# Kernel tuning notes

Hardware: AMD Instinct MI355X
Metric: run time of the kernel (lower is better)

## Reference

```python
import jax, jax.numpy as jnp
import numpy as np

EMB_DIM = 1024
N_HEAD = 16
HEAD_SIZE = 64
B = 2
T = 2048


def setup_inputs() -> dict:
    key = jax.random.key(0)
    k_x, k_qkv, k_pw, k_pb = jax.random.split(key, 4)
    x = jax.random.normal(k_x, (B, T, EMB_DIM), dtype=jnp.float32)
    # nn.Linear(emb_dim, 3*emb_dim, bias=False): y = x @ W_qkv, W_qkv: [C, 3C]
    W_qkv = jax.random.normal(k_qkv, (EMB_DIM, 3 * EMB_DIM), dtype=jnp.float32) * (EMB_DIM ** -0.5)
    # nn.Linear(emb_dim, emb_dim) with bias
    W_proj = jax.random.normal(k_pw, (EMB_DIM, EMB_DIM), dtype=jnp.float32) * (EMB_DIM ** -0.5)
    b_proj = jax.random.normal(k_pb, (EMB_DIM,), dtype=jnp.float32) * 0.01
    return {"x": x, "W_qkv": W_qkv, "W_proj": W_proj, "b_proj": b_proj}


def reference(x, W_qkv, W_proj, b_proj):
    Bn, Tn, C = x.shape
    qkv = x @ W_qkv                          # [B, T, 3C]
    q, k, v = jnp.split(qkv, 3, axis=-1)
    # [B, T, H, D] -> attention over heads via einsum (no explicit transpose)
    q = q.reshape(Bn, Tn, N_HEAD, HEAD_SIZE)
    k = k.reshape(Bn, Tn, N_HEAD, HEAD_SIZE)
    v = v.reshape(Bn, Tn, N_HEAD, HEAD_SIZE)
    att = jnp.einsum("bthd,bshd->bhts", q, k) * (HEAD_SIZE ** -0.5)  # [B, H, T, T]
    causal = jnp.tril(jnp.ones((Tn, Tn), dtype=bool))
    att = jnp.where(causal, att, -jnp.inf)
    att = jax.nn.softmax(att, axis=-1)
    y = jnp.einsum("bhts,bshd->bthd", att, v).reshape(Bn, Tn, C)
    return y @ W_proj + b_proj
```

## Files before the change

kernel.cpp:

```cpp
#include <hip/hip_runtime.h>
#include <hip/hip_bf16.h>

typedef unsigned short u16;
typedef unsigned int u32;
typedef u16 u16x4 __attribute__((ext_vector_type(4)));
typedef u16 u16x8 __attribute__((ext_vector_type(8)));
typedef u32 u32x4 __attribute__((ext_vector_type(4)));
typedef __bf16 bf16x8 __attribute__((ext_vector_type(8)));
typedef float f32x4 __attribute__((ext_vector_type(4)));

__device__ __forceinline__ u16 f2bf(float f) {
  union { float f; unsigned u; } v; v.f = f;
  unsigned r = v.u + 0x7fffu + ((v.u >> 16) & 1u);
  return (u16)(r >> 16);
}

__device__ __forceinline__ u16 bf(float f) {
  __bf16 h = (__bf16)f;
  union { __bf16 h; u16 u; } c; c.h = h;
  return c.u;
}

__device__ __forceinline__ u32 pack2(float lo, float hi) {
  return (u32)bf(lo) | ((u32)bf(hi) << 16);
}

__device__ __forceinline__ float fexp2(float x) {
#if __has_builtin(__builtin_amdgcn_exp2f)
  return __builtin_amdgcn_exp2f(x);
#else
  return exp2f(x);
#endif
}

__device__ __forceinline__ float frcp(float x) {
#if __has_builtin(__builtin_amdgcn_rcpf)
  return __builtin_amdgcn_rcpf(x);
#else
  return 1.0f / x;
#endif
}

__device__ __forceinline__ void gload16(const void* g, void* l) {
  __builtin_amdgcn_global_load_lds((const __attribute__((address_space(1))) void*)g,
                                   (__attribute__((address_space(3))) void*)l, 16, 0, 0);
}

__global__ __launch_bounds__(256) void cvt_bf16(const float* __restrict__ in,
                                                u16* __restrict__ out, int n) {
  int i = (blockIdx.x * 256 + threadIdx.x) * 8;
  if (i >= n) return;
  f32x4 a = *(const f32x4*)(in + i);
  f32x4 b = *(const f32x4*)(in + i + 4);
  u16x8 r;
  r[0] = f2bf(a[0]); r[1] = f2bf(a[1]); r[2] = f2bf(a[2]); r[3] = f2bf(a[3]);
  r[4] = f2bf(b[0]); r[5] = f2bf(b[1]); r[6] = f2bf(b[2]); r[7] = f2bf(b[3]);
  *(u16x8*)(out + i) = r;
}

__global__ __launch_bounds__(256) void transpose_w(
    const float* __restrict__ Wqkv, const float* __restrict__ Wproj,
    u16* __restrict__ wqT, u16* __restrict__ wpT)
{
  __shared__ float tile[32][33];
  int bx = blockIdx.x;
  const float* in;
  u16* out;
  int N;
  if (bx < 96) { in = Wqkv; out = wqT; N = 3072; }
  else         { in = Wproj; out = wpT; N = 1024; bx -= 96; }
  const int K = 1024;
  int n0 = bx * 32, k0 = blockIdx.y * 32;
  int tx = threadIdx.x & 31, ty = threadIdx.x >> 5;
  for (int i = 0; i < 32; i += 8)
    tile[ty + i][tx] = in[(long)(k0 + ty + i) * N + n0 + tx];
  __syncthreads();
  for (int i = 0; i < 32; i += 8)
    out[(long)(n0 + ty + i) * K + k0 + tx] = f2bf(tile[tx][ty + i]);
}

template<int BM, int BN, bool F32OUT>
__global__ __launch_bounds__(256) void gemm_bt(
    const u16* __restrict__ A, const u16* __restrict__ Bt,
    void* __restrict__ Cp, const float* __restrict__ bias,
    int M, int N, int K)
{
  constexpr int MR = BM / 32, NR = BN / 32;
  constexpr int RA = BM / 32, RB = BN / 32;
  __shared__ char lds[(BM + BN) * 128];
  char* As = lds;
  char* Bs = lds + BM * 128;
  const int tid = threadIdx.x;
  const int l = tid & 63, w = tid >> 6;
  const int wr = w >> 1, wc = w & 1;
  const int lr = l & 15, q4 = l >> 4;
  const long row0 = (long)blockIdx.x * BM;
  const long col0 = (long)blockIdx.y * BN;

  f32x4 acc[MR][NR] = {};

  const u16* gA[RA];
  int oA[RA];
  for (int i = 0; i < RA; ++i) {
    int cc = i * 256 + tid;
    int r = cc >> 3, c = (cc & 7) ^ (r & 7);
    oA[i] = cc * 16;
    gA[i] = A + (row0 + r) * K + c * 8;
  }
  const u16* gB[RB];
  int oB[RB];
  for (int i = 0; i < RB; ++i) {
    int cc = i * 256 + tid;
    int r = cc >> 3, c = (cc & 7) ^ (r & 7);
    oB[i] = cc * 16;
    gB[i] = Bt + (col0 + r) * K + c * 8;
  }

  for (int k0 = 0; k0 < K; k0 += 64) {
    __syncthreads();
    for (int i = 0; i < RA; ++i) gload16(gA[i] + k0, As + oA[i]);
    for (int i = 0; i < RB; ++i) gload16(gB[i] + k0, Bs + oB[i]);
    __syncthreads();
    for (int kk = 0; kk < 2; ++kk) {
      bf16x8 a[MR], b[NR];
      for (int m = 0; m < MR; ++m) {
        int r = wr * (BM / 2) + m * 16 + lr;
        a[m] = *(const bf16x8*)(As + r * 128 + (((kk * 4 + q4) ^ (r & 7)) << 4));
      }
      for (int n = 0; n < NR; ++n) {
        int r = wc * (BN / 2) + n * 16 + lr;
        b[n] = *(const bf16x8*)(Bs + r * 128 + (((kk * 4 + q4) ^ (r & 7)) << 4));
      }
      for (int m = 0; m < MR; ++m)
        for (int n = 0; n < NR; ++n)
          acc[m][n] = __builtin_amdgcn_mfma_f32_16x16x32_bf16(a[m], b[n], acc[m][n], 0, 0, 0);
    }
  }

  for (int n = 0; n < NR; ++n) {
    int col = (int)col0 + wc * (BN / 2) + n * 16 + lr;
    float bv = 0.f;
    if (F32OUT) bv = bias[col];
    for (int m = 0; m < MR; ++m) {
      for (int reg = 0; reg < 4; ++reg) {
        long row = row0 + wr * (BM / 2) + m * 16 + q4 * 4 + reg;
        float vv = acc[m][n][reg] + bv;
        if (F32OUT) ((float*)Cp)[row * N + col] = vv;
        else        ((u16*)Cp)[row * N + col] = f2bf(vv);
      }
    }
  }
}

#define FXOR(d) (((((d) & 7) ^ (((d) >> 3) & 7))) << 4)

#define VSCAT(vtb, ra, rb)                                                     \
  for (int j = 0; j < 4; ++j) {                                                \
    int d = vd0 + j;                                                           \
    *(u32*)((vtb) + d * 128 + (vcol2 ^ FXOR(d))) = (u32)(ra)[j] | ((u32)(rb)[j] << 16); \
  }

#define COMPUTE_TILE(T)                                                        \
  if (64 * (T) <= wrow + 15) {                                                 \
    char* ks_ = ksmem + ((T) & 3) * 8192;                                      \
    char* vt_ = vtmem + ((T) & 3) * 8192;                                      \
    const int k0_ = 64 * (T);                                                  \
    f32x4 st[4] = {};                                                          \
    __builtin_amdgcn_s_setprio(1);                                             \
    for (int kk = 0; kk < 2; ++kk)                                             \
      for (int n = 0; n < 4; ++n) {                                            \
        int r = n * 16 + lr;                                                   \
        int c = (kk * 4 + g) ^ (r & 7);                                        \
        bf16x8 kf = *(const bf16x8*)(ks_ + r * 128 + (c << 4));                \
        st[n] = __builtin_amdgcn_mfma_f32_16x16x32_bf16(kf, qf[kk], st[n], 0, 0, 0); \
      }                                                                        \
    __builtin_amdgcn_s_setprio(0);                                             \
    if (k0_ + 63 > wrow) {                                                     \
      for (int n = 0; n < 4; ++n)                                              \
        for (int reg = 0; reg < 4; ++reg)                                      \
          if (k0_ + n * 16 + g * 4 + reg > wrow + lr)                          \
            st[n][reg] = -__builtin_inff();                                    \
    }                                                                          \
    float pm = fmaxf(fmaxf(fmaxf(st[0][0], st[0][1]), fmaxf(st[0][2], st[0][3])), \
                     fmaxf(fmaxf(st[1][0], st[1][1]), fmaxf(st[1][2], st[1][3]))); \
    pm = fmaxf(pm, fmaxf(fmaxf(fmaxf(st[2][0], st[2][1]), fmaxf(st[2][2], st[2][3])), \
                         fmaxf(fmaxf(st[3][0], st[3][1]), fmaxf(st[3][2], st[3][3])))); \
    pm = fmaxf(pm, __shfl_xor(pm, 16));                                        \
    pm = fmaxf(pm, __shfl_xor(pm, 32));                                        \
    if (__any(pm > mrun + 8.f)) {                                              \
      float mn = fmaxf(mrun, pm);                                              \
      float scl = fexp2(mrun - mn);                                            \
      mrun = mn;                                                               \
      lsum *= scl;                                                             \
      for (int n = 0; n < 4; ++n)                                              \
        for (int reg = 0; reg < 4; ++reg) o[n][reg] *= scl;                    \
    }                                                                          \
    float psum = 0.f;                                                          \
    u32 pk[4][2];                                                              \
    for (int n = 0; n < 4; ++n) {                                              \
      float p0 = fexp2(st[n][0] - mrun), p1 = fexp2(st[n][1] - mrun);          \
      float p2 = fexp2(st[n][2] - mrun), p3 = fexp2(st[n][3] - mrun);          \
      psum += (p0 + p1) + (p2 + p3);                                           \
      pk[n][0] = pack2(p0, p1);                                                \
      pk[n][1] = pack2(p2, p3);                                                \
    }                                                                          \
    lsum += psum;                                                              \
    __builtin_amdgcn_s_setprio(1);                                             \
    for (int kt = 0; kt < 2; ++kt) {                                           \
      u32x4 pb;                                                                \
      pb[0] = pk[2 * kt][0]; pb[1] = pk[2 * kt][1];                            \
      pb[2] = pk[2 * kt + 1][0]; pb[3] = pk[2 * kt + 1][1];                    \
      bf16x8 pf = *(bf16x8*)&pb;                                               \
      for (int n = 0; n < 4; ++n) {                                            \
        int dd = n * 16 + lr;                                                  \
        bf16x8 vf = *(const bf16x8*)(vt_ + dd * 128 + ((kt * 64 + g * 16) ^ FXOR(dd))); \
        o[n] = __builtin_amdgcn_mfma_f32_16x16x32_bf16(vf, pf, o[n], 0, 0, 0); \
      }                                                                        \
    }                                                                          \
    __builtin_amdgcn_s_setprio(0);                                             \
  }

__global__ __launch_bounds__(512) void attn_fwd(
    const u16* __restrict__ qkv, u16* __restrict__ atty)
{
  __shared__ char ksmem[4 * 8192];
  __shared__ char vtmem[4 * 8192];
  const int tid = threadIdx.x;
  const int l = tid & 63, w = tid >> 6;
  const int lr = l & 15, g = l >> 4;
  const int h = blockIdx.y;
  const int ti = blockIdx.x;
  const long base = (long)blockIdx.z * 2048;
  const int wrow = (w < 4) ? (ti * 64 + w * 16) : ((31 - ti) * 64 + (w - 4) * 16);

  bf16x8 qf[2];
  for (int kk = 0; kk < 2; ++kk) {
    u16x8 raw = *(const u16x8*)(qkv + (base + wrow + lr) * 3072 + h * 64 + kk * 32 + g * 8);
    u16x8 sc;
    for (int j = 0; j < 8; ++j) {
      union { unsigned u; float f; } c; c.u = ((unsigned)raw[j]) << 16;
      sc[j] = bf(c.f * 0.18033688f);
    }
    qf[kk] = *(bf16x8*)&sc;
  }

  float mrun = -__builtin_inff(), lsum = 0.f;
  f32x4 o[4] = {};

  const int kr = tid >> 3, kc = (tid & 7) ^ (kr & 7);
  const u16* kg = qkv + (base + kr) * 3072 + 1024 + h * 64 + kc * 8;
  const int va = tid >> 4;
  const int vd0 = (tid & 15) * 4;
  const int vk0 = va * 2;
  const int vn = vk0 >> 4, vgp2 = (vk0 >> 2) & 3, vr = vk0 & 3;
  const int vcol2 = ((vn >> 1) * 32 + vgp2 * 8 + (vn & 1) * 4 + vr) * 2;
  const u16* vgp = qkv + (base + vk0) * 3072 + 2048 + h * 64 + vd0;

  const int nkv = 32 - ti;

  {
    u16x4 a0 = *(const u16x4*)(vgp);
    u16x4 b0 = *(const u16x4*)(vgp + 3072);
    u16x4 a1 = *(const u16x4*)(vgp + 196608);
    u16x4 b1 = *(const u16x4*)(vgp + 196608 + 3072);
    gload16(kg, ksmem + tid * 16);
    gload16(kg + 196608, ksmem + 8192 + tid * 16);
    VSCAT(vtmem, a0, b0);
    VSCAT(vtmem + 8192, a1, b1);
  }
  __syncthreads();

  for (int tb = 0; tb < nkv; tb += 2) {
    u16x4 p2a, p2b, p3a, p3b;
    const bool pf2 = (tb + 2) < nkv, pf3 = (tb + 3) < nkv;
    if (pf2) {
      long off = (long)(tb + 2) * 196608;
      p2a = *(const u16x4*)(vgp + off);
      p2b = *(const u16x4*)(vgp + off + 3072);
      gload16(kg + off, ksmem + ((tb + 2) & 3) * 8192 + tid * 16);
    }
    if (pf3) {
      long off = (long)(tb + 3) * 196608;
      p3a = *(const u16x4*)(vgp + off);
      p3b = *(const u16x4*)(vgp + off + 3072);
      gload16(kg + off, ksmem + ((tb + 3) & 3) * 8192 + tid * 16);
    }

    COMPUTE_TILE(tb);
    if (tb + 1 < nkv) COMPUTE_TILE(tb + 1);

    if (pf2) VSCAT(vtmem + ((tb + 2) & 3) * 8192, p2a, p2b);
    if (pf3) VSCAT(vtmem + ((tb + 3) & 3) * 8192, p3a, p3b);
    __syncthreads();
  }

  lsum += __shfl_xor(lsum, 16);
  lsum += __shfl_xor(lsum, 32);
  float inv = frcp(lsum);
  long row = base + wrow + lr;
  for (int n = 0; n < 4; ++n) {
    u16x4 ov;
    for (int reg = 0; reg < 4; ++reg) ov[reg] = bf(o[n][reg] * inv);
    *(u16x4*)(atty + row * 1024 + h * 64 + n * 16 + g * 4) = ov;
  }
}

extern "C" void kernel_launch(void* const* d_in, const int* in_sizes, int n_in,
                              void* d_out, int out_size, void* d_ws, size_t ws_size,
                              hipStream_t stream) {
  const float* x     = (const float*)d_in[0];
  const float* Wqkv  = (const float*)d_in[1];
  const float* Wproj = (const float*)d_in[2];
  const float* bproj = (const float*)d_in[3];
  char* ws = (char*)d_ws;
  u16* xb   = (u16*)(ws);
  u16* wqT  = (u16*)(ws + 8388608);
  u16* wpT  = (u16*)(ws + 14680064);
  u16* qkv  = (u16*)(ws + 16777216);
  u16* atty = (u16*)(ws + 41943040);

  cvt_bf16<<<2048, 256, 0, stream>>>(x, xb, 4194304);
  transpose_w<<<dim3(128, 32), 256, 0, stream>>>(Wqkv, Wproj, wqT, wpT);
  gemm_bt<128, 128, false><<<dim3(32, 24), 256, 0, stream>>>(xb, wqT, (void*)qkv, nullptr, 4096, 3072, 1024);
  attn_fwd<<<dim3(16, 16, 2), 512, 0, stream>>>(qkv, atty);
  gemm_bt<128, 64, true><<<dim3(32, 16), 256, 0, stream>>>(atty, wpT, d_out, bproj, 4096, 1024, 1024);
}
```

Measured before the change: 114.0 us.

## Switch attention kernel to 32x32x16 MFMA with 4 waves of 32 query rows

Rewrites the flash-attention inner loop to use 32x32x16 bf16 MFMA instead of 16x16x32, with each wave owning 32 query rows and the block shrinking from 8 to 4 waves. K and V staging is widened so each thread loads two K rows and eight V columns, and the V scatter permutation is rebuilt to match the new fragment layout. The aim is fewer MFMA issues and less LDS fragment traffic per FLOP. In exchange each wave holds more registers, and fewer waves per block can reduce latency hiding.

```diff
diff --git a/kernel.cpp b/kernel.cpp
--- a/kernel.cpp
+++ b/kernel.cpp
@@ -8,6 +8,7 @@
 typedef u32 u32x4 __attribute__((ext_vector_type(4)));
 typedef __bf16 bf16x8 __attribute__((ext_vector_type(8)));
 typedef float f32x4 __attribute__((ext_vector_type(4)));
+typedef float f32x16 __attribute__((ext_vector_type(16)));
 
 __device__ __forceinline__ u16 f2bf(float f) {
   union { float f; unsigned u; } v; v.f = f;
@@ -155,135 +156,158 @@
 #define FXOR(d) (((((d) & 7) ^ (((d) >> 3) & 7))) << 4)
 
 #define VSCAT(vtb, ra, rb)                                                     \
-  for (int j = 0; j < 4; ++j) {                                                \
+  _Pragma("unroll")                                                            \
+  for (int j = 0; j < 8; ++j) {                                                \
     int d = vd0 + j;                                                           \
     *(u32*)((vtb) + d * 128 + (vcol2 ^ FXOR(d))) = (u32)(ra)[j] | ((u32)(rb)[j] << 16); \
   }
 
 #define COMPUTE_TILE(T)                                                        \
-  if (64 * (T) <= wrow + 15) {                                                 \
+  if ((T) <= tw) {                                                             \
     char* ks_ = ksmem + ((T) & 3) * 8192;                                      \
     char* vt_ = vtmem + ((T) & 3) * 8192;                                      \
-    const int k0_ = 64 * (T);                                                  \
-    f32x4 st[4] = {};                                                          \
+    f32x16 st[2] = {};                                                         \
     __builtin_amdgcn_s_setprio(1);                                             \
-    for (int kk = 0; kk < 2; ++kk)                                             \
-      for (int n = 0; n < 4; ++n) {                                            \
-        int r = n * 16 + lr;                                                   \
-        int c = (kk * 4 + g) ^ (r & 7);                                        \
-        bf16x8 kf = *(const bf16x8*)(ks_ + r * 128 + (c << 4));                \
-        st[n] = __builtin_amdgcn_mfma_f32_16x16x32_bf16(kf, qf[kk], st[n], 0, 0, 0); \
+    _Pragma("unroll")                                                          \
+    for (int w2 = 0; w2 < 2; ++w2) {                                           \
+      _Pragma("unroll")                                                        \
+      for (int sub = 0; sub < 4; ++sub) {                                      \
+        int r = w2 * 32 + lq;                                                  \
+        bf16x8 kf = *(const bf16x8*)(ks_ + r * 128 + (((sub * 2 + hi) ^ (r & 7)) << 4)); \
+        st[w2] = __builtin_amdgcn_mfma_f32_32x32x16_bf16(kf, qf[sub], st[w2], 0, 0, 0); \
       }                                                                        \
+    }                                                                          \
     __builtin_amdgcn_s_setprio(0);                                             \
-    if (k0_ + 63 > wrow) {                                                     \
-      for (int n = 0; n < 4; ++n)                                              \
-        for (int reg = 0; reg < 4; ++reg)                                      \
-          if (k0_ + n * 16 + g * 4 + reg > wrow + lr)                          \
-            st[n][reg] = -__builtin_inff();                                    \
-    }                                                                          \
-    float pm = fmaxf(fmaxf(fmaxf(st[0][0], st[0][1]), fmaxf(st[0][2], st[0][3])), \
-                     fmaxf(fmaxf(st[1][0], st[1][1]), fmaxf(st[1][2], st[1][3]))); \
-    pm = fmaxf(pm, fmaxf(fmaxf(fmaxf(st[2][0], st[2][1]), fmaxf(st[2][2], st[2][3])), \
-                         fmaxf(fmaxf(st[3][0], st[3][1]), fmaxf(st[3][2], st[3][3])))); \
-    pm = fmaxf(pm, __shfl_xor(pm, 16));                                        \
+    if ((T) == tw) {                                                           \
+      const int ro = (wrow & 32) + lq;                                         \
+      _Pragma("unroll")                                                        \
+      for (int w2 = 0; w2 < 2; ++w2)                                           \
+        _Pragma("unroll")                                                      \
+        for (int r = 0; r < 16; ++r)                                           \
+          if (w2 * 32 + (r & 3) + 8 * (r >> 2) + 4 * hi > ro)                  \
+            st[w2][r] = -__builtin_inff();                                     \
+    }                                                                          \
+    float pm = st[0][0];                                                       \
+    _Pragma("unroll")                                                          \
+    for (int r = 1; r < 16; ++r) pm = fmaxf(pm, st[0][r]);                     \
+    _Pragma("unroll")                                                          \
+    for (int r = 0; r < 16; ++r) pm = fmaxf(pm, st[1][r]);                     \
     pm = fmaxf(pm, __shfl_xor(pm, 32));                                        \
     if (__any(pm > mrun + 8.f)) {                                              \
       float mn = fmaxf(mrun, pm);                                              \
       float scl = fexp2(mrun - mn);                                            \
       mrun = mn;                                                               \
       lsum *= scl;                                                             \
-      for (int n = 0; n < 4; ++n)                                              \
-        for (int reg = 0; reg < 4; ++reg) o[n][reg] *= scl;                    \
-    }                                                                          \
+      _Pragma("unroll")                                                        \
+      for (int w2 = 0; w2 < 2; ++w2)                                           \
+        _Pragma("unroll")                                                      \
+        for (int r = 0; r < 16; ++r) o[w2][r] *= scl;                          \
+    }                                                                          \
+    u32 pk[2][8];                                                              \
     float psum = 0.f;                                                          \
-    u32 pk[4][2];                                                              \
-    for (int n = 0; n < 4; ++n) {                                              \
-      float p0 = fexp2(st[n][0] - mrun), p1 = fexp2(st[n][1] - mrun);          \
-      float p2 = fexp2(st[n][2] - mrun), p3 = fexp2(st[n][3] - mrun);          \
-      psum += (p0 + p1) + (p2 + p3);                                           \
-      pk[n][0] = pack2(p0, p1);                                                \
-      pk[n][1] = pack2(p2, p3);                                                \
+    _Pragma("unroll")                                                          \
+    for (int w2 = 0; w2 < 2; ++w2) {                                           \
+      _Pragma("unroll")                                                        \
+      for (int i2 = 0; i2 < 8; ++i2) {                                         \
+        float p0 = fexp2(st[w2][2 * i2] - mrun);                               \
+        float p1 = fexp2(st[w2][2 * i2 + 1] - mrun);                           \
+        psum += p0 + p1;                                                       \
+        pk[w2][i2] = pack2(p0, p1);                                            \
+      }                                                                        \
     }                                                                          \
     lsum += psum;                                                              \
     __builtin_amdgcn_s_setprio(1);                                             \
-    for (int kt = 0; kt < 2; ++kt) {                                           \
-      u32x4 pb;                                                                \
-      pb[0] = pk[2 * kt][0]; pb[1] = pk[2 * kt][1];                            \
-      pb[2] = pk[2 * kt + 1][0]; pb[3] = pk[2 * kt + 1][1];                    \
-      bf16x8 pf = *(bf16x8*)&pb;                                               \
-      for (int n = 0; n < 4; ++n) {                                            \
-        int dd = n * 16 + lr;                                                  \
-        bf16x8 vf = *(const bf16x8*)(vt_ + dd * 128 + ((kt * 64 + g * 16) ^ FXOR(dd))); \
-        o[n] = __builtin_amdgcn_mfma_f32_16x16x32_bf16(vf, pf, o[n], 0, 0, 0); \
+    _Pragma("unroll")                                                          \
+    for (int w2 = 0; w2 < 2; ++w2) {                                           \
+      _Pragma("unroll")                                                        \
+      for (int kt = 0; kt < 2; ++kt) {                                         \
+        u32x4 pbu = {pk[w2][4 * kt], pk[w2][4 * kt + 1],                       \
+                     pk[w2][4 * kt + 2], pk[w2][4 * kt + 3]};                  \
+        bf16x8 pf = *(bf16x8*)&pbu;                                            \
+        _Pragma("unroll")                                                      \
+        for (int dt = 0; dt < 2; ++dt) {                                       \
+          int dr = dt * 32 + lq;                                               \
+          bf16x8 vf = *(const bf16x8*)(vt_ + dr * 128 +                        \
+                        (((w2 * 64 + kt * 32 + hi * 16)) ^ FXOR(dr)));         \
+          o[dt] = __builtin_amdgcn_mfma_f32_32x32x16_bf16(vf, pf, o[dt], 0, 0, 0); \
+        }                                                                      \
       }                                                                        \
     }                                                                          \
     __builtin_amdgcn_s_setprio(0);                                             \
   }
 
-__global__ __launch_bounds__(512) void attn_fwd(
+__global__ __launch_bounds__(256) void attn_fwd(
     const u16* __restrict__ qkv, u16* __restrict__ atty)
 {
   __shared__ char ksmem[4 * 8192];
   __shared__ char vtmem[4 * 8192];
   const int tid = threadIdx.x;
   const int l = tid & 63, w = tid >> 6;
-  const int lr = l & 15, g = l >> 4;
+  const int lq = l & 31, hi = l >> 5;
   const int h = blockIdx.y;
   const int ti = blockIdx.x;
   const long base = (long)blockIdx.z * 2048;
-  const int wrow = (w < 4) ? (ti * 64 + w * 16) : ((31 - ti) * 64 + (w - 4) * 16);
-
-  bf16x8 qf[2];
-  for (int kk = 0; kk < 2; ++kk) {
-    u16x8 raw = *(const u16x8*)(qkv + (base + wrow + lr) * 3072 + h * 64 + kk * 32 + g * 8);
+  const int wrow = (w < 2) ? (ti * 64 + w * 32) : ((31 - ti) * 64 + (w - 2) * 32);
+  const int tw = wrow >> 6;
+
+  bf16x8 qf[4];
+  for (int sub = 0; sub < 4; ++sub) {
+    u16x8 raw = *(const u16x8*)(qkv + (base + wrow + lq) * 3072 + h * 64 + sub * 16 + hi * 8);
     u16x8 sc;
     for (int j = 0; j < 8; ++j) {
       union { unsigned u; float f; } c; c.u = ((unsigned)raw[j]) << 16;
       sc[j] = bf(c.f * 0.18033688f);
     }
-    qf[kk] = *(bf16x8*)&sc;
+    qf[sub] = *(bf16x8*)&sc;
   }
 
   float mrun = -__builtin_inff(), lsum = 0.f;
-  f32x4 o[4] = {};
-
-  const int kr = tid >> 3, kc = (tid & 7) ^ (kr & 7);
-  const u16* kg = qkv + (base + kr) * 3072 + 1024 + h * 64 + kc * 8;
-  const int va = tid >> 4;
-  const int vd0 = (tid & 15) * 4;
+  f32x16 o[2] = {};
+
+  const int kr0 = tid >> 3, kc0 = (tid & 7) ^ (kr0 & 7);
+  const int kr1 = 32 + kr0, kc1 = (tid & 7) ^ (kr1 & 7);
+  const u16* kg0 = qkv + (base + kr0) * 3072 + 1024 + h * 64 + kc0 * 8;
+  const u16* kg1 = qkv + (base + kr1) * 3072 + 1024 + h * 64 + kc1 * 8;
+  const int va = tid & 31;
+  const int vd0 = (tid >> 5) * 8;
   const int vk0 = va * 2;
-  const int vn = vk0 >> 4, vgp2 = (vk0 >> 2) & 3, vr = vk0 & 3;
-  const int vcol2 = ((vn >> 1) * 32 + vgp2 * 8 + (vn & 1) * 4 + vr) * 2;
+  const int vq = (vk0 >> 2) & 3;
+  const int vpos = vk0 + (vq == 1 ? 4 : (vq == 2 ? -4 : 0));
+  const int vcol2 = vpos * 2;
   const u16* vgp = qkv + (base + vk0) * 3072 + 2048 + h * 64 + vd0;
 
   const int nkv = 32 - ti;
 
   {
-    u16x4 a0 = *(const u16x4*)(vgp);
-    u16x4 b0 = *(const u16x4*)(vgp + 3072);
-    u16x4 a1 = *(const u16x4*)(vgp + 196608);
-    u16x4 b1 = *(const u16x4*)(vgp + 196608 + 3072);
-    gload16(kg, ksmem + tid * 16);
-    gload16(kg + 196608, ksmem + 8192 + tid * 16);
+    u16x8 a0 = *(const u16x8*)(vgp);
+    u16x8 b0 = *(const u16x8*)(vgp + 3072);
+    u16x8 a1 = *(const u16x8*)(vgp + 196608);
+    u16x8 b1 = *(const u16x8*)(vgp + 196608 + 3072);
+    gload16(kg0, ksmem + tid * 16);
+    gload16(kg1, ksmem + 4096 + tid * 16);
+    gload16(kg0 + 196608, ksmem + 8192 + tid * 16);
+    gload16(kg1 + 196608, ksmem + 8192 + 4096 + tid * 16);
     VSCAT(vtmem, a0, b0);
     VSCAT(vtmem + 8192, a1, b1);
   }
   __syncthreads();
 
   for (int tb = 0; tb < nkv; tb += 2) {
-    u16x4 p2a, p2b, p3a, p3b;
+    u16x8 p2a, p2b, p3a, p3b;
     const bool pf2 = (tb + 2) < nkv, pf3 = (tb + 3) < nkv;
     if (pf2) {
       long off = (long)(tb + 2) * 196608;
-      p2a = *(const u16x4*)(vgp + off);
-      p2b = *(const u16x4*)(vgp + off + 3072);
-      gload16(kg + off, ksmem + ((tb + 2) & 3) * 8192 + tid * 16);
+      p2a = *(const u16x8*)(vgp + off);
+      p2b = *(const u16x8*)(vgp + off + 3072);
+      gload16(kg0 + off, ksmem + ((tb + 2) & 3) * 8192 + tid * 16);
+      gload16(kg1 + off, ksmem + ((tb + 2) & 3) * 8192 + 4096 + tid * 16);
     }
     if (pf3) {
       long off = (long)(tb + 3) * 196608;
-      p3a = *(const u16x4*)(vgp + off);
-      p3b = *(const u16x4*)(vgp + off + 3072);
-      gload16(kg + off, ksmem + ((tb + 3) & 3) * 8192 + tid * 16);
+      p3a = *(const u16x8*)(vgp + off);
+      p3b = *(const u16x8*)(vgp + off + 3072);
+      gload16(kg0 + off, ksmem + ((tb + 3) & 3) * 8192 + tid * 16);
+      gload16(kg1 + off, ksmem + ((tb + 3) & 3) * 8192 + 4096 + tid * 16);
     }
 
     COMPUTE_TILE(tb);
@@ -294,14 +318,15 @@
     __syncthreads();
   }
 
-  lsum += __shfl_xor(lsum, 16);
   lsum += __shfl_xor(lsum, 32);
   float inv = frcp(lsum);
-  long row = base + wrow + lr;
-  for (int n = 0; n < 4; ++n) {
-    u16x4 ov;
-    for (int reg = 0; reg < 4; ++reg) ov[reg] = bf(o[n][reg] * inv);
-    *(u16x4*)(atty + row * 1024 + h * 64 + n * 16 + g * 4) = ov;
+  long row = base + wrow + lq;
+  for (int dt = 0; dt < 2; ++dt) {
+    for (int rg = 0; rg < 4; ++rg) {
+      u16x4 ov;
+      for (int e = 0; e < 4; ++e) ov[e] = bf(o[dt][rg * 4 + e] * inv);
+      *(u16x4*)(atty + row * 1024 + h * 64 + dt * 32 + rg * 8 + hi * 4) = ov;
+    }
   }
 }
 
@@ -322,6 +347,6 @@
   cvt_bf16<<<2048, 256, 0, stream>>>(x, xb, 4194304);
   transpose_w<<<dim3(128, 32), 256, 0, stream>>>(Wqkv, Wproj, wqT, wpT);
   gemm_bt<128, 128, false><<<dim3(32, 24), 256, 0, stream>>>(xb, wqT, (void*)qkv, nullptr, 4096, 3072, 1024);
-  attn_fwd<<<dim3(16, 16, 2), 512, 0, stream>>>(qkv, atty);
+  attn_fwd<<<dim3(16, 16, 2), 256, 0, stream>>>(qkv, atty);
   gemm_bt<128, 64, true><<<dim3(32, 16), 256, 0, stream>>>(atty, wpT, d_out, bproj, 4096, 1024, 1024);
 }
```

New measurement: 134.5 us. 18.0% more time.
